# Kernel optimization log

Measured on AMD Instinct MI355X. Metric: run time of the kernel, lower is better.

Reference implementation:

```python
import jax, jax.numpy as jnp
import numpy as np

B, N, C = 4, 8192, 64

def setup_inputs() -> dict:
    key = jax.random.key(0)
    ks = jax.random.split(key, 9)
    s = 1.0 / np.sqrt(C)
    x = jax.random.normal(ks[0], (B, N, C), dtype=jnp.float32)
    # Linear params: weight [C_out, C_in] (torch convention), bias [C_out]
    Wq = jax.random.uniform(ks[1], (C, C), jnp.float32, -s, s)
    bq = jax.random.uniform(ks[2], (C,), jnp.float32, -s, s)
    Wk = jax.random.uniform(ks[3], (C, C), jnp.float32, -s, s)
    bk = jax.random.uniform(ks[4], (C,), jnp.float32, -s, s)
    Wv = jax.random.uniform(ks[5], (C, C), jnp.float32, -s, s)
    bv = jax.random.uniform(ks[6], (C,), jnp.float32, -s, s)
    Ww = jax.random.uniform(ks[7], (C, C), jnp.float32, -s, s)
    bw = jax.random.uniform(ks[8], (C,), jnp.float32, -s, s)
    return {"x": x, "Wq": Wq, "bq": bq, "Wk": Wk, "bk": bk,
            "Wv": Wv, "bv": bv, "Ww": Ww, "bw": bw}

def reference(x, Wq, bq, Wk, bk, Wv, bv, Ww, bw):
    # x: [B, N, C]
    q = jnp.einsum('bnc,dc->bnd', x, Wq) + bq
    k = jnp.einsum('bnc,dc->bnd', x, Wk) + bk
    v = jnp.einsum('bnc,dc->bnd', x, Wv) + bv
    C_ = x.shape[-1]
    N_ = x.shape[1]
    # kernel = q @ k^T / sqrt(C); integral = kernel @ v / N  (no softmax)
    kernel = jnp.einsum('bnd,bmd->bnm', q, k) / jnp.sqrt(jnp.float32(C_))
    integral = jnp.einsum('bnm,bmd->bnd', kernel, v) / N_
    w_x = jnp.einsum('bnc,dc->bnd', x, Ww) + bw
    return jax.nn.gelu(w_x + integral, approximate=False)
```

## Files before the change

### kernel.cpp

```cpp
#include <hip/hip_runtime.h>
#include <stdint.h>

typedef unsigned int u32;
typedef unsigned short u16;
typedef short short8 __attribute__((ext_vector_type(8)));
typedef float f32x16 __attribute__((ext_vector_type(16)));

#define BN 8192
#define NPB 32
#define NT 4

__device__ __forceinline__ u32 f2b_u(float f){
  u32 x = __float_as_uint(f);
  return (x + 0x7fffu + ((x >> 16) & 1u)) >> 16;
}
__device__ __forceinline__ float b2f(u16 h){
  return __uint_as_float(((u32)h) << 16);
}
__device__ __forceinline__ float gelu_exact(float v){
  return 0.5f * v * (1.0f + erff(v * 0.70710678118654752440f));
}
__device__ __forceinline__ void add4(float4& a, const float4 b){
  a.x += b.x; a.y += b.y; a.z += b.z; a.w += b.w;
}

__global__ __launch_bounds__(256) void k_gram(const float* __restrict__ x,
                                              float* __restrict__ part){
  int bid = blockIdx.x;
  int b = bid >> 5, blk = bid & (NPB - 1);
  int t = threadIdx.x, w = t >> 6, lane = t & 63;
  const float* xb = x + (size_t)b * BN * 64 + (size_t)blk * 256 * 64;

  __shared__ __align__(16) u16 xT[64][72];
  __shared__ float mred[256][16];

  int wi = w >> 1, wj = w & 1;
  int r = t >> 2, cg = t & 3;

  f32x16 acc;
  #pragma unroll
  for (int i = 0; i < 16; ++i) acc[i] = 0.f;
  float macc[16];
  #pragma unroll
  for (int j = 0; j < 16; ++j) macc[j] = 0.f;

  for (int tile = 0; tile < NT; ++tile){
    const float4* src = (const float4*)(xb + ((size_t)(tile * 64 + r)) * 64 + cg * 16);
    float4 v0 = src[0], v1 = src[1], v2 = src[2], v3 = src[3];
    float vv[16] = { v0.x, v0.y, v0.z, v0.w,  v1.x, v1.y, v1.z, v1.w,
                     v2.x, v2.y, v2.z, v2.w,  v3.x, v3.y, v3.z, v3.w };
    #pragma unroll
    for (int j = 0; j < 16; ++j){
      macc[j] += vv[j];
      xT[cg * 16 + j][r] = (u16)f2b_u(vv[j]);
    }
    __syncthreads();

    #pragma unroll
    for (int ks = 0; ks < 4; ++ks){
      int n0 = ks * 16 + (lane >> 5) * 8;
      short8 af = *(const short8*)&xT[wi * 32 + (lane & 31)][n0];
      short8 bf = *(const short8*)&xT[wj * 32 + (lane & 31)][n0];
      acc = __builtin_amdgcn_mfma_f32_32x32x16_bf16(af, bf, acc, 0, 0, 0);
    }
    __syncthreads();
  }

  float* dst = part + (size_t)bid * 4160;
  #pragma unroll
  for (int q = 0; q < 16; ++q){
    int grow = wi * 32 + (q & 3) + 8 * (q >> 2) + 4 * (lane >> 5);
    dst[grow * 64 + wj * 32 + (lane & 31)] = acc[q];
  }

  #pragma unroll
  for (int j = 0; j < 16; ++j) mred[t][j] = macc[j];
  __syncthreads();
  if (t < 64){
    int cgc = t >> 4, j = t & 15;
    float s0 = 0.f, s1 = 0.f, s2 = 0.f, s3 = 0.f;
    for (int ss = 0; ss < 64; ss += 4){
      s0 += mred[cgc + 4 * ss][j];
      s1 += mred[cgc + 4 * (ss + 1)][j];
      s2 += mred[cgc + 4 * (ss + 2)][j];
      s3 += mred[cgc + 4 * (ss + 3)][j];
    }
    dst[4096 + t] = (s0 + s1) + (s2 + s3);
  }
}

__global__ __launch_bounds__(64) void k_reduceW(const float4* __restrict__ part4,
                                                float4* __restrict__ Gred4){
  int blk = blockIdx.x;
  int b = blk / 65, chunk = blk - b * 65;
  int t = threadIdx.x;
  int e4 = chunk * 16 + (t & 15);
  int pg = t >> 4;

  __shared__ float4 red[4][16];

  const float4* base = part4 + (size_t)b * NPB * 1040 + e4;
  float4 s = make_float4(0.f, 0.f, 0.f, 0.f);
  #pragma unroll
  for (int p = 0; p < 8; ++p)
    add4(s, base[(size_t)(pg * 8 + p) * 1040]);
  red[pg][t & 15] = s;
  __syncthreads();

  if (t < 16){
    float4 a = red[0][t], c = red[1][t];
    add4(a, red[2][t]);
    add4(c, red[3][t]);
    add4(a, c);
    Gred4[(size_t)b * 1040 + chunk * 16 + t] = a;
  }
}

__global__ __launch_bounds__(256) void k_combineM(
    const float* __restrict__ Gred,
    const float* __restrict__ Wq, const float* __restrict__ bq,
    const float* __restrict__ Wk, const float* __restrict__ bk,
    const float* __restrict__ Wv, const float* __restrict__ bv,
    const float* __restrict__ Ww, const float* __restrict__ bw,
    u16* __restrict__ Mws, float* __restrict__ biasws)
{
  int b = blockIdx.x;
  int t = threadIdx.x, w = t >> 6, lane = t & 63;
  int wi = w >> 1, wj = w & 1;
  int r = t >> 2, cg = t & 3;

  __shared__ __align__(16) u16 G16[64][72];
  __shared__ __align__(16) u16 Wk16[64][72];
  __shared__ __align__(16) u16 Wv16[64][72];
  __shared__ __align__(16) u16 WqT16[64][72];
  __shared__ __align__(16) u16 T16[64][72];
  __shared__ __align__(16) u16 St16[64][72];
  __shared__ float mrow[72];
  __shared__ float Tcol64[64];
  __shared__ float bkl[64], bvl[64], bql[64];

  const float* Gb = Gred + (size_t)b * 4160;

  {
    const float4* s4 = (const float4*)(Gb + r * 64 + cg * 16);
    float4 a0 = s4[0], a1 = s4[1], a2 = s4[2], a3 = s4[3];
    float vv[16] = { a0.x,a0.y,a0.z,a0.w, a1.x,a1.y,a1.z,a1.w,
                     a2.x,a2.y,a2.z,a2.w, a3.x,a3.y,a3.z,a3.w };
    #pragma unroll
    for (int j = 0; j < 8; ++j)
      *(u32*)&G16[r][cg * 16 + 2*j] = f2b_u(vv[2*j]) | (f2b_u(vv[2*j+1]) << 16);
  }
  {
    const float4* s4 = (const float4*)(Wk + r * 64 + cg * 16);
    float4 a0 = s4[0], a1 = s4[1], a2 = s4[2], a3 = s4[3];
    float vv[16] = { a0.x,a0.y,a0.z,a0.w, a1.x,a1.y,a1.z,a1.w,
                     a2.x,a2.y,a2.z,a2.w, a3.x,a3.y,a3.z,a3.w };
    #pragma unroll
    for (int j = 0; j < 8; ++j)
      *(u32*)&Wk16[r][cg * 16 + 2*j] = f2b_u(vv[2*j]) | (f2b_u(vv[2*j+1]) << 16);
  }
  {
    const float4* s4 = (const float4*)(Wv + r * 64 + cg * 16);
    float4 a0 = s4[0], a1 = s4[1], a2 = s4[2], a3 = s4[3];
    float vv[16] = { a0.x,a0.y,a0.z,a0.w, a1.x,a1.y,a1.z,a1.w,
                     a2.x,a2.y,a2.z,a2.w, a3.x,a3.y,a3.z,a3.w };
    #pragma unroll
    for (int j = 0; j < 8; ++j)
      *(u32*)&Wv16[r][cg * 16 + 2*j] = f2b_u(vv[2*j]) | (f2b_u(vv[2*j+1]) << 16);
  }
  {
    const float4* s4 = (const float4*)(Wq + r * 64 + cg * 16);
    float4 a0 = s4[0], a1 = s4[1], a2 = s4[2], a3 = s4[3];
    float vv[16] = { a0.x,a0.y,a0.z,a0.w, a1.x,a1.y,a1.z,a1.w,
                     a2.x,a2.y,a2.z,a2.w, a3.x,a3.y,a3.z,a3.w };
    #pragma unroll
    for (int j = 0; j < 16; ++j)
      WqT16[cg * 16 + j][r] = (u16)f2b_u(vv[j]);
  }
  if (t < 64){
    mrow[t] = Gb[4096 + t];
    bkl[t] = bk[t];
    bvl[t] = bv[t];
    bql[t] = bq[t];
  }
  if (t == 0) mrow[64] = (float)BN;
  __syncthreads();

  {
    f32x16 tf;
    #pragma unroll
    for (int i = 0; i < 16; ++i) tf[i] = 0.f;
    #pragma unroll
    for (int ks = 0; ks < 4; ++ks){
      int n0 = ks * 16 + (lane >> 5) * 8;
      short8 af = *(const short8*)&Wk16[wi * 32 + (lane & 31)][n0];
      short8 bf = *(const short8*)&G16 [wj * 32 + (lane & 31)][n0];
      tf = __builtin_amdgcn_mfma_f32_32x32x16_bf16(af, bf, tf, 0, 0, 0);
    }
    int c = wj * 32 + (lane & 31);
    float mc = mrow[c];
    #pragma unroll
    for (int q = 0; q < 16; ++q){
      int i = wi * 32 + (q & 3) + 8 * (q >> 2) + 4 * (lane >> 5);
      T16[i][c] = (u16)f2b_u(tf[q] + bkl[i] * mc);
    }
    if (w == 0){
      float s = 0.f;
      for (int a = 0; a < 64; ++a) s = fmaf(b2f(Wk16[lane][a]), mrow[a], s);
      Tcol64[lane] = fmaf(bkl[lane], (float)BN, s);
    }
  }
  __syncthreads();

  {
    f32x16 sf;
    #pragma unroll
    for (int i = 0; i < 16; ++i) sf[i] = 0.f;
    #pragma unroll
    for (int ks = 0; ks < 4; ++ks){
      int n0 = ks * 16 + (lane >> 5) * 8;
      short8 af = *(const short8*)&T16 [wi * 32 + (lane & 31)][n0];
      short8 bf = *(const short8*)&Wv16[wj * 32 + (lane & 31)][n0];
      sf = __builtin_amdgcn_mfma_f32_32x32x16_bf16(af, bf, sf, 0, 0, 0);
    }
    int j = wj * 32 + (lane & 31);
    float bvj = bvl[j];
    #pragma unroll
    for (int q = 0; q < 16; ++q){
      int i = wi * 32 + (q & 3) + 8 * (q >> 2) + 4 * (lane >> 5);
      St16[j][i] = (u16)f2b_u(sf[q] + Tcol64[i] * bvj);
    }
  }
  __syncthreads();

  {
    const float inv = 1.0f / 65536.0f;
    f32x16 mf;
    #pragma unroll
    for (int i = 0; i < 16; ++i) mf[i] = 0.f;
    #pragma unroll
    for (int ks = 0; ks < 4; ++ks){
      int n0 = ks * 16 + (lane >> 5) * 8;
      short8 af = *(const short8*)&St16 [wi * 32 + (lane & 31)][n0];
      short8 bf = *(const short8*)&WqT16[wj * 32 + (lane & 31)][n0];
      mf = __builtin_amdgcn_mfma_f32_32x32x16_bf16(af, bf, mf, 0, 0, 0);
    }
    int c = wj * 32 + (lane & 31);
    u16* Mb = Mws + (size_t)b * 4608;
    #pragma unroll
    for (int q = 0; q < 16; ++q){
      int d = wi * 32 + (q & 3) + 8 * (q >> 2) + 4 * (lane >> 5);
      float val = fmaf(inv, mf[q], Ww[d * 64 + c]);
      Mb[d * 72 + c] = (u16)f2b_u(val);
    }
    if (w == 0){
      float s = 0.f;
      for (int e = 0; e < 64; ++e) s = fmaf(b2f(St16[lane][e]), bql[e], s);
      biasws[b * 64 + lane] = fmaf(inv, s, bw[lane]);
    }
  }
}

__global__ __launch_bounds__(256) void k_out(const float* __restrict__ x,
                                             const u32* __restrict__ Mws,
                                             const float* __restrict__ biasws,
                                             float* __restrict__ out)
{
  int bid = blockIdx.x;
  int b = bid >> 7, blk = bid & 127;
  int t = threadIdx.x, w = t >> 6, lane = t & 63;
  int rowbase = blk * 64;

  __shared__ __align__(16) u16 Mb16[64][72];
  __shared__ __align__(16) u16 xR[64][72];
  __shared__ float Mbias[64];

  {
    const u32* Msrc = Mws + (size_t)b * 2304;
    u32* Mdst = (u32*)&Mb16[0][0];
    #pragma unroll
    for (int i = 0; i < 9; ++i) Mdst[t + 256 * i] = Msrc[t + 256 * i];
    if (t < 64) Mbias[t] = biasws[b * 64 + t];
  }

  {
    int r = t >> 2, cg = t & 3;
    const float4* src = (const float4*)(x + ((size_t)b * BN + rowbase + r) * 64 + cg * 16);
    float4 v0 = src[0], v1 = src[1], v2 = src[2], v3 = src[3];
    float vv[16] = { v0.x, v0.y, v0.z, v0.w,  v1.x, v1.y, v1.z, v1.w,
                     v2.x, v2.y, v2.z, v2.w,  v3.x, v3.y, v3.z, v3.w };
    #pragma unroll
    for (int j = 0; j < 8; ++j){
      u32 pk = f2b_u(vv[2*j]) | (f2b_u(vv[2*j+1]) << 16);
      *(u32*)&xR[r][cg * 16 + 2*j] = pk;
    }
  }
  __syncthreads();

  int wi = w >> 1, wj = w & 1;
  f32x16 oacc;
  #pragma unroll
  for (int i = 0; i < 16; ++i) oacc[i] = 0.f;
  #pragma unroll
  for (int ks = 0; ks < 4; ++ks){
    int c0 = ks * 16 + (lane >> 5) * 8;
    short8 af = *(const short8*)&xR  [wi * 32 + (lane & 31)][c0];
    short8 bf = *(const short8*)&Mb16[wj * 32 + (lane & 31)][c0];
    oacc = __builtin_amdgcn_mfma_f32_32x32x16_bf16(af, bf, oacc, 0, 0, 0);
  }

  float bias_v = Mbias[wj * 32 + (lane & 31)];
  int d = wj * 32 + (lane & 31);
  #pragma unroll
  for (int q = 0; q < 16; ++q){
    int n = rowbase + wi * 32 + (q & 3) + 8 * (q >> 2) + 4 * (lane >> 5);
    out[((size_t)b * BN + n) * 64 + d] = gelu_exact(oacc[q] + bias_v);
  }
}

extern "C" void kernel_launch(void* const* d_in, const int* in_sizes, int n_in,
                              void* d_out, int out_size, void* d_ws, size_t ws_size,
                              hipStream_t stream) {
  const float* x  = (const float*)d_in[0];
  const float* Wq = (const float*)d_in[1];
  const float* bq = (const float*)d_in[2];
  const float* Wk = (const float*)d_in[3];
  const float* bk = (const float*)d_in[4];
  const float* Wv = (const float*)d_in[5];
  const float* bv = (const float*)d_in[6];
  const float* Ww = (const float*)d_in[7];
  const float* bw = (const float*)d_in[8];
  float* out = (float*)d_out;

  float* ws     = (float*)d_ws;
  float* part   = ws;
  float* Gred   = ws + 532480;
  u16*   Mws    = (u16*)(ws + 549120);
  float* biasws = ws + 549120 + 9216;

  k_gram    <<<dim3(4 * NPB), 256, 0, stream>>>(x, part);
  k_reduceW <<<dim3(260),      64, 0, stream>>>((const float4*)part, (float4*)Gred);
  k_combineM<<<dim3(4),       256, 0, stream>>>(Gred, Wq, bq, Wk, bk,
                                                Wv, bv, Ww, bw, Mws, biasws);
  k_out     <<<dim3(512),     256, 0, stream>>>(x, (const u32*)Mws, biasws, out);
}
```

Baseline: 22.87 us.

## Fuse combine-M into output kernel with redundant per-block compute; double gram blocks

Removes the tiny 4-block k_combineM launch by having each of the 512 output blocks recompute the 64x64 combined matrix M and bias from the reduced Gram statistics in shared memory, aliasing the two phases' buffers through a union. The x tile load is issued early so it overlaps the M computation. Separately, the Gram pass now uses 64 partial blocks per batch of 128 rows each instead of 32 blocks of 256, giving more parallelism at the cost of a larger reduction. This trades one launch and a serial stage for redundant work of three small MFMA chains per block, plus higher shared memory use that may reduce occupancy.

```diff
diff --git a/kernel.cpp b/kernel.cpp
--- a/kernel.cpp
+++ b/kernel.cpp
@@ -7,8 +7,8 @@
 typedef float f32x16 __attribute__((ext_vector_type(16)));
 
 #define BN 8192
-#define NPB 32
-#define NT 4
+#define NPB 64
+#define NT 2
 
 __device__ __forceinline__ u32 f2b_u(float f){
   u32 x = __float_as_uint(f);
@@ -27,9 +27,9 @@
 __global__ __launch_bounds__(256) void k_gram(const float* __restrict__ x,
                                               float* __restrict__ part){
   int bid = blockIdx.x;
-  int b = bid >> 5, blk = bid & (NPB - 1);
+  int b = bid >> 6, blk = bid & (NPB - 1);
   int t = threadIdx.x, w = t >> 6, lane = t & 63;
-  const float* xb = x + (size_t)b * BN * 64 + (size_t)blk * 256 * 64;
+  const float* xb = x + (size_t)b * BN * 64 + (size_t)blk * 128 * 64;
 
   __shared__ __align__(16) u16 xT[64][72];
   __shared__ float mred[256][16];
@@ -102,8 +102,8 @@
   const float4* base = part4 + (size_t)b * NPB * 1040 + e4;
   float4 s = make_float4(0.f, 0.f, 0.f, 0.f);
   #pragma unroll
-  for (int p = 0; p < 8; ++p)
-    add4(s, base[(size_t)(pg * 8 + p) * 1040]);
+  for (int p = 0; p < 16; ++p)
+    add4(s, base[(size_t)(pg * 16 + p) * 1040]);
   red[pg][t & 15] = s;
   __syncthreads();
 
@@ -116,28 +116,33 @@
   }
 }
 
-__global__ __launch_bounds__(256) void k_combineM(
-    const float* __restrict__ Gred,
+union SMX {
+  struct {
+    u16 G16[64][72]; u16 Wk16[64][72]; u16 Wv16[64][72]; u16 WqT16[64][72];
+    u16 T16[64][72]; u16 St16[64][72];
+    float mrow[72]; float Tcol64[64]; float bkl[64], bvl[64], bql[64];
+  } c;
+  struct { u16 Mb16[64][72]; u16 xR[64][72]; float Mbias[64]; } o;
+};
+
+__global__ __launch_bounds__(256) void k_outcM(
+    const float* __restrict__ x, const float* __restrict__ Gred,
     const float* __restrict__ Wq, const float* __restrict__ bq,
     const float* __restrict__ Wk, const float* __restrict__ bk,
     const float* __restrict__ Wv, const float* __restrict__ bv,
     const float* __restrict__ Ww, const float* __restrict__ bw,
-    u16* __restrict__ Mws, float* __restrict__ biasws)
+    float* __restrict__ out)
 {
-  int b = blockIdx.x;
+  __shared__ SMX sm;
+  int bid = blockIdx.x;
+  int b = bid >> 7, blk = bid & 127;
   int t = threadIdx.x, w = t >> 6, lane = t & 63;
   int wi = w >> 1, wj = w & 1;
   int r = t >> 2, cg = t & 3;
-
-  __shared__ __align__(16) u16 G16[64][72];
-  __shared__ __align__(16) u16 Wk16[64][72];
-  __shared__ __align__(16) u16 Wv16[64][72];
-  __shared__ __align__(16) u16 WqT16[64][72];
-  __shared__ __align__(16) u16 T16[64][72];
-  __shared__ __align__(16) u16 St16[64][72];
-  __shared__ float mrow[72];
-  __shared__ float Tcol64[64];
-  __shared__ float bkl[64], bvl[64], bql[64];
+  int rowbase = blk * 64;
+
+  const float4* xsrc = (const float4*)(x + ((size_t)b * BN + rowbase + r) * 64 + cg * 16);
+  float4 xv0 = xsrc[0], xv1 = xsrc[1], xv2 = xsrc[2], xv3 = xsrc[3];
 
   const float* Gb = Gred + (size_t)b * 4160;
 
@@ -148,7 +153,7 @@
                      a2.x,a2.y,a2.z,a2.w, a3.x,a3.y,a3.z,a3.w };
     #pragma unroll
     for (int j = 0; j < 8; ++j)
-      *(u32*)&G16[r][cg * 16 + 2*j] = f2b_u(vv[2*j]) | (f2b_u(vv[2*j+1]) << 16);
+      *(u32*)&sm.c.G16[r][cg * 16 + 2*j] = f2b_u(vv[2*j]) | (f2b_u(vv[2*j+1]) << 16);
   }
   {
     const float4* s4 = (const float4*)(Wk + r * 64 + cg * 16);
@@ -157,7 +162,7 @@
                      a2.x,a2.y,a2.z,a2.w, a3.x,a3.y,a3.z,a3.w };
     #pragma unroll
     for (int j = 0; j < 8; ++j)
-      *(u32*)&Wk16[r][cg * 16 + 2*j] = f2b_u(vv[2*j]) | (f2b_u(vv[2*j+1]) << 16);
+      *(u32*)&sm.c.Wk16[r][cg * 16 + 2*j] = f2b_u(vv[2*j]) | (f2b_u(vv[2*j+1]) << 16);
   }
   {
     const float4* s4 = (const float4*)(Wv + r * 64 + cg * 16);
@@ -166,7 +171,7 @@
                      a2.x,a2.y,a2.z,a2.w, a3.x,a3.y,a3.z,a3.w };
     #pragma unroll
     for (int j = 0; j < 8; ++j)
-      *(u32*)&Wv16[r][cg * 16 + 2*j] = f2b_u(vv[2*j]) | (f2b_u(vv[2*j+1]) << 16);
+      *(u32*)&sm.c.Wv16[r][cg * 16 + 2*j] = f2b_u(vv[2*j]) | (f2b_u(vv[2*j+1]) << 16);
   }
   {
     const float4* s4 = (const float4*)(Wq + r * 64 + cg * 16);
@@ -175,15 +180,15 @@
                      a2.x,a2.y,a2.z,a2.w, a3.x,a3.y,a3.z,a3.w };
     #pragma unroll
     for (int j = 0; j < 16; ++j)
-      WqT16[cg * 16 + j][r] = (u16)f2b_u(vv[j]);
+      sm.c.WqT16[cg * 16 + j][r] = (u16)f2b_u(vv[j]);
   }
   if (t < 64){
-    mrow[t] = Gb[4096 + t];
-    bkl[t] = bk[t];
-    bvl[t] = bv[t];
-    bql[t] = bq[t];
-  }
-  if (t == 0) mrow[64] = (float)BN;
+    sm.c.mrow[t] = Gb[4096 + t];
+    sm.c.bkl[t] = bk[t];
+    sm.c.bvl[t] = bv[t];
+    sm.c.bql[t] = bq[t];
+  }
+  if (t == 0) sm.c.mrow[64] = (float)BN;
   __syncthreads();
 
   {
@@ -193,21 +198,21 @@
     #pragma unroll
     for (int ks = 0; ks < 4; ++ks){
       int n0 = ks * 16 + (lane >> 5) * 8;
-      short8 af = *(const short8*)&Wk16[wi * 32 + (lane & 31)][n0];
-      short8 bf = *(const short8*)&G16 [wj * 32 + (lane & 31)][n0];
+      short8 af = *(const short8*)&sm.c.Wk16[wi * 32 + (lane & 31)][n0];
+      short8 bf = *(const short8*)&sm.c.G16 [wj * 32 + (lane & 31)][n0];
       tf = __builtin_amdgcn_mfma_f32_32x32x16_bf16(af, bf, tf, 0, 0, 0);
     }
     int c = wj * 32 + (lane & 31);
-    float mc = mrow[c];
+    float mc = sm.c.mrow[c];
     #pragma unroll
     for (int q = 0; q < 16; ++q){
       int i = wi * 32 + (q & 3) + 8 * (q >> 2) + 4 * (lane >> 5);
-      T16[i][c] = (u16)f2b_u(tf[q] + bkl[i] * mc);
+      sm.c.T16[i][c] = (u16)f2b_u(tf[q] + sm.c.bkl[i] * mc);
     }
     if (w == 0){
       float s = 0.f;
-      for (int a = 0; a < 64; ++a) s = fmaf(b2f(Wk16[lane][a]), mrow[a], s);
-      Tcol64[lane] = fmaf(bkl[lane], (float)BN, s);
+      for (int a = 0; a < 64; ++a) s = fmaf(b2f(sm.c.Wk16[lane][a]), sm.c.mrow[a], s);
+      sm.c.Tcol64[lane] = fmaf(sm.c.bkl[lane], (float)BN, s);
     }
   }
   __syncthreads();
@@ -219,16 +224,16 @@
     #pragma unroll
     for (int ks = 0; ks < 4; ++ks){
       int n0 = ks * 16 + (lane >> 5) * 8;
-      short8 af = *(const short8*)&T16 [wi * 32 + (lane & 31)][n0];
-      short8 bf = *(const short8*)&Wv16[wj * 32 + (lane & 31)][n0];
+      short8 af = *(const short8*)&sm.c.T16 [wi * 32 + (lane & 31)][n0];
+      short8 bf = *(const short8*)&sm.c.Wv16[wj * 32 + (lane & 31)][n0];
       sf = __builtin_amdgcn_mfma_f32_32x32x16_bf16(af, bf, sf, 0, 0, 0);
     }
     int j = wj * 32 + (lane & 31);
-    float bvj = bvl[j];
+    float bvj = sm.c.bvl[j];
     #pragma unroll
     for (int q = 0; q < 16; ++q){
       int i = wi * 32 + (q & 3) + 8 * (q >> 2) + 4 * (lane >> 5);
-      St16[j][i] = (u16)f2b_u(sf[q] + Tcol64[i] * bvj);
+      sm.c.St16[j][i] = (u16)f2b_u(sf[q] + sm.c.Tcol64[i] * bvj);
     }
   }
   __syncthreads();
@@ -241,80 +246,54 @@
     #pragma unroll
     for (int ks = 0; ks < 4; ++ks){
       int n0 = ks * 16 + (lane >> 5) * 8;
-      short8 af = *(const short8*)&St16 [wi * 32 + (lane & 31)][n0];
-      short8 bf = *(const short8*)&WqT16[wj * 32 + (lane & 31)][n0];
+      short8 af = *(const short8*)&sm.c.St16 [wi * 32 + (lane & 31)][n0];
+      short8 bf = *(const short8*)&sm.c.WqT16[wj * 32 + (lane & 31)][n0];
       mf = __builtin_amdgcn_mfma_f32_32x32x16_bf16(af, bf, mf, 0, 0, 0);
     }
     int c = wj * 32 + (lane & 31);
-    u16* Mb = Mws + (size_t)b * 4608;
     #pragma unroll
     for (int q = 0; q < 16; ++q){
       int d = wi * 32 + (q & 3) + 8 * (q >> 2) + 4 * (lane >> 5);
       float val = fmaf(inv, mf[q], Ww[d * 64 + c]);
-      Mb[d * 72 + c] = (u16)f2b_u(val);
+      sm.o.Mb16[d][c] = (u16)f2b_u(val);
     }
     if (w == 0){
       float s = 0.f;
-      for (int e = 0; e < 64; ++e) s = fmaf(b2f(St16[lane][e]), bql[e], s);
-      biasws[b * 64 + lane] = fmaf(inv, s, bw[lane]);
-    }
-  }
-}
-
-__global__ __launch_bounds__(256) void k_out(const float* __restrict__ x,
-                                             const u32* __restrict__ Mws,
-                                             const float* __restrict__ biasws,
-                                             float* __restrict__ out)
-{
-  int bid = blockIdx.x;
-  int b = bid >> 7, blk = bid & 127;
-  int t = threadIdx.x, w = t >> 6, lane = t & 63;
-  int rowbase = blk * 64;
-
-  __shared__ __align__(16) u16 Mb16[64][72];
-  __shared__ __align__(16) u16 xR[64][72];
-  __shared__ float Mbias[64];
-
-  {
-    const u32* Msrc = Mws + (size_t)b * 2304;
-    u32* Mdst = (u32*)&Mb16[0][0];
-    #pragma unroll
-    for (int i = 0; i < 9; ++i) Mdst[t + 256 * i] = Msrc[t + 256 * i];
-    if (t < 64) Mbias[t] = biasws[b * 64 + t];
-  }
-
-  {
-    int r = t >> 2, cg = t & 3;
-    const float4* src = (const float4*)(x + ((size_t)b * BN + rowbase + r) * 64 + cg * 16);
-    float4 v0 = src[0], v1 = src[1], v2 = src[2], v3 = src[3];
-    float vv[16] = { v0.x, v0.y, v0.z, v0.w,  v1.x, v1.y, v1.z, v1.w,
-                     v2.x, v2.y, v2.z, v2.w,  v3.x, v3.y, v3.z, v3.w };
+      for (int e = 0; e < 64; ++e) s = fmaf(b2f(sm.c.St16[lane][e]), sm.c.bql[e], s);
+      sm.o.Mbias[lane] = fmaf(inv, s, bw[lane]);
+    }
+  }
+
+  {
+    float vv[16] = { xv0.x, xv0.y, xv0.z, xv0.w,  xv1.x, xv1.y, xv1.z, xv1.w,
+                     xv2.x, xv2.y, xv2.z, xv2.w,  xv3.x, xv3.y, xv3.z, xv3.w };
     #pragma unroll
     for (int j = 0; j < 8; ++j){
       u32 pk = f2b_u(vv[2*j]) | (f2b_u(vv[2*j+1]) << 16);
-      *(u32*)&xR[r][cg * 16 + 2*j] = pk;
-    }
-  }
-  __syncthreads();
-
-  int wi = w >> 1, wj = w & 1;
-  f32x16 oacc;
-  #pragma unroll
-  for (int i = 0; i < 16; ++i) oacc[i] = 0.f;
-  #pragma unroll
-  for (int ks = 0; ks < 4; ++ks){
-    int c0 = ks * 16 + (lane >> 5) * 8;
-    short8 af = *(const short8*)&xR  [wi * 32 + (lane & 31)][c0];
-    short8 bf = *(const short8*)&Mb16[wj * 32 + (lane & 31)][c0];
-    oacc = __builtin_amdgcn_mfma_f32_32x32x16_bf16(af, bf, oacc, 0, 0, 0);
-  }
-
-  float bias_v = Mbias[wj * 32 + (lane & 31)];
-  int d = wj * 32 + (lane & 31);
-  #pragma unroll
-  for (int q = 0; q < 16; ++q){
-    int n = rowbase + wi * 32 + (q & 3) + 8 * (q >> 2) + 4 * (lane >> 5);
-    out[((size_t)b * BN + n) * 64 + d] = gelu_exact(oacc[q] + bias_v);
+      *(u32*)&sm.o.xR[r][cg * 16 + 2*j] = pk;
+    }
+  }
+  __syncthreads();
+
+  {
+    f32x16 oacc;
+    #pragma unroll
+    for (int i = 0; i < 16; ++i) oacc[i] = 0.f;
+    #pragma unroll
+    for (int ks = 0; ks < 4; ++ks){
+      int c0 = ks * 16 + (lane >> 5) * 8;
+      short8 af = *(const short8*)&sm.o.xR  [wi * 32 + (lane & 31)][c0];
+      short8 bf = *(const short8*)&sm.o.Mb16[wj * 32 + (lane & 31)][c0];
+      oacc = __builtin_amdgcn_mfma_f32_32x32x16_bf16(af, bf, oacc, 0, 0, 0);
+    }
+
+    float bias_v = sm.o.Mbias[wj * 32 + (lane & 31)];
+    int d = wj * 32 + (lane & 31);
+    #pragma unroll
+    for (int q = 0; q < 16; ++q){
+      int n = rowbase + wi * 32 + (q & 3) + 8 * (q >> 2) + 4 * (lane >> 5);
+      out[((size_t)b * BN + n) * 64 + d] = gelu_exact(oacc[q] + bias_v);
+    }
   }
 }
 
@@ -332,15 +311,12 @@
   const float* bw = (const float*)d_in[8];
   float* out = (float*)d_out;
 
-  float* ws     = (float*)d_ws;
-  float* part   = ws;
-  float* Gred   = ws + 532480;
-  u16*   Mws    = (u16*)(ws + 549120);
-  float* biasws = ws + 549120 + 9216;
-
-  k_gram    <<<dim3(4 * NPB), 256, 0, stream>>>(x, part);
-  k_reduceW <<<dim3(260),      64, 0, stream>>>((const float4*)part, (float4*)Gred);
-  k_combineM<<<dim3(4),       256, 0, stream>>>(Gred, Wq, bq, Wk, bk,
-                                                Wv, bv, Ww, bw, Mws, biasws);
-  k_out     <<<dim3(512),     256, 0, stream>>>(x, (const u32*)Mws, biasws, out);
-}
+  float* ws   = (float*)d_ws;
+  float* part = ws;
+  float* Gred = ws + 1064960;
+
+  k_gram   <<<dim3(4 * NPB), 256, 0, stream>>>(x, part);
+  k_reduceW<<<dim3(260),      64, 0, stream>>>((const float4*)part, (float4*)Gred);
+  k_outcM  <<<dim3(512),     256, 0, stream>>>(x, Gred, Wq, bq, Wk, bk,
+                                               Wv, bv, Ww, bw, out);
+}
```

Result: slower. 26.53 us (+16.0%).
